# Performance work log

Measured on AMD Instinct MI355X. Metric: run time of the kernel, lower is better.

## Reference

```python
import jax, jax.numpy as jnp
import numpy as np

N_NODES = 10000
IN_CH = 512
HID = 128
HEADS = 4
OUT_CH = 256
N_EDGES = 160000
NEG_SLOPE = 0.2  # PyG GATConv default


def gat_conv(x, src, dst, W, a_src, a_dst, b):
    """PyG-style GATConv. x:[N,F_in], W:[F_in,H*C], a_src/a_dst:[H,C], b:[H*C].
    src/dst already include self-loops. Returns [N, H*C] (concat heads)."""
    N = x.shape[0]
    H, C = a_src.shape
    h = (x @ W).reshape(N, H, C)                     # [N,H,C]
    e_src = jnp.einsum('nhc,hc->nh', h, a_src)        # [N,H]
    e_dst = jnp.einsum('nhc,hc->nh', h, a_dst)
    alpha = jax.nn.leaky_relu(e_src[src] + e_dst[dst], NEG_SLOPE)  # [E,H]
    # softmax over incoming edges of each destination node
    m = jax.ops.segment_max(alpha, dst, num_segments=N)            # [N,H]
    ex = jnp.exp(alpha - m[dst])
    denom = jax.ops.segment_sum(ex, dst, num_segments=N)           # [N,H]
    coeff = ex / (denom[dst] + 1e-16)                              # [E,H]
    out = jax.ops.segment_sum(coeff[:, :, None] * h[src], dst, num_segments=N)  # [N,H,C]
    return out.reshape(N, H * C) + b


def _edges_with_self_loops(edge_index, n):
    loops = jnp.arange(n, dtype=edge_index.dtype)
    src = jnp.concatenate([edge_index[0], loops])
    dst = jnp.concatenate([edge_index[1], loops])
    return src, dst


def setup_inputs() -> dict:
    key = jax.random.key(0)
    ks = jax.random.split(key, 20)
    s = 0.05
    inp = {
        'x': jax.random.normal(ks[0], (N_NODES, IN_CH), jnp.float32),
        'W1': jax.random.normal(ks[1], (IN_CH, HEADS * HID), jnp.float32) * s,
        'a1s': jax.random.normal(ks[2], (HEADS, HID), jnp.float32) * s,
        'a1d': jax.random.normal(ks[3], (HEADS, HID), jnp.float32) * s,
        'b1': jnp.zeros((HEADS * HID,), jnp.float32),
        'W2': jax.random.normal(ks[4], (HEADS * HID, HEADS * HID), jnp.float32) * s,
        'a2s': jax.random.normal(ks[5], (HEADS, HID), jnp.float32) * s,
        'a2d': jax.random.normal(ks[6], (HEADS, HID), jnp.float32) * s,
        'b2': jnp.zeros((HEADS * HID,), jnp.float32),
        'W3': jax.random.normal(ks[7], (HEADS * HID, HID), jnp.float32) * s,
        'a3s': jax.random.normal(ks[8], (1, HID), jnp.float32) * s,
        'a3d': jax.random.normal(ks[9], (1, HID), jnp.float32) * s,
        'b3': jnp.zeros((HID,), jnp.float32),
        'Wl': jax.random.normal(ks[10], (HID, OUT_CH), jnp.float32) * s,
        'bl': jnp.zeros((OUT_CH,), jnp.float32),
        'Wr': jax.random.normal(ks[11], (IN_CH, OUT_CH), jnp.float32) * s,
        'br': jnp.zeros((OUT_CH,), jnp.float32),
        'edge_index': jax.random.randint(ks[12], (2, N_EDGES), 0, N_NODES, jnp.int64 if jax.config.jax_enable_x64 else jnp.int32),
    }
    return inp


def reference(x, W1, a1s, a1d, b1, W2, a2s, a2d, b2, W3, a3s, a3d, b3, Wl, bl, Wr, br, edge_index):
    src, dst = _edges_with_self_loops(edge_index, x.shape[0])
    residual = x @ Wr + br
    h = jax.nn.elu(gat_conv(x, src, dst, W1, a1s, a1d, b1))
    h = jax.nn.elu(gat_conv(h, src, dst, W2, a2s, a2d, b2))
    h = jax.nn.elu(gat_conv(h, src, dst, W3, a3s, a3d, b3))
    return h @ Wl + bl + residual
```

## Files before the change

kernel.cpp:

```cpp
#include <hip/hip_runtime.h>
#include <hip/hip_bf16.h>
#include <cstdint>
#include <cstddef>

#define N_NODES 10000
#define M_PAD   10112
#define HEADS   4

typedef __bf16 bfrag8 __attribute__((ext_vector_type(8)));
typedef __bf16 bfrag2 __attribute__((ext_vector_type(2)));
typedef float  floatx4 __attribute__((ext_vector_type(4)));
typedef float  floatx2 __attribute__((ext_vector_type(2)));

#define S0V (M_PAD * 512 / 8)
#define S1 (512 * 512)
#define S2 (512 * 512)
#define S3 (512 * 128)
#define S4 (128 * 256)
#define S5 (512 * 256)

__global__ __launch_bounds__(256) void prep(const float* __restrict__ x,
                                            const float* __restrict__ W1,
                                            const float* __restrict__ W2,
                                            const float* __restrict__ W3,
                                            const float* __restrict__ Wl,
                                            const float* __restrict__ Wr,
                                            const int* __restrict__ edst, int E,
                                            __bf16* __restrict__ xb,
                                            __bf16* __restrict__ W1T,
                                            __bf16* __restrict__ W2T,
                                            __bf16* __restrict__ W3T,
                                            __bf16* __restrict__ WlT,
                                            __bf16* __restrict__ WrT,
                                            int* __restrict__ deg) {
    int i = blockIdx.x * 256 + threadIdx.x;
    if (i < S0V) {
        int base = i * 8;
        int row = base >> 9;
        bfrag8 r = {};
        if (row < N_NODES) {
            float4 f0 = ((const float4*)x)[i * 2];
            float4 f1 = ((const float4*)x)[i * 2 + 1];
            r[0] = (__bf16)f0.x; r[1] = (__bf16)f0.y; r[2] = (__bf16)f0.z; r[3] = (__bf16)f0.w;
            r[4] = (__bf16)f1.x; r[5] = (__bf16)f1.y; r[6] = (__bf16)f1.z; r[7] = (__bf16)f1.w;
        }
        *(bfrag8*)(xb + base) = r;
    } else if ((i -= S0V) < S1) {
        int k = i >> 9, n = i & 511;
        W1T[n * 512 + k] = (__bf16)W1[i];
    } else if ((i -= S1) < S2) {
        int k = i >> 9, n = i & 511;
        W2T[n * 512 + k] = (__bf16)W2[i];
    } else if ((i -= S2) < S3) {
        int k = i >> 7, n = i & 127;
        W3T[n * 512 + k] = (__bf16)W3[i];
    } else if ((i -= S3) < S4) {
        int k = i >> 8, n = i & 255;
        WlT[n * 128 + k] = (__bf16)Wl[i];
    } else if ((i -= S4) < S5) {
        int k = i >> 8, n = i & 255;
        WrT[n * 512 + k] = (__bf16)Wr[i];
    } else if ((i -= S5) < E) {
        atomicAdd(&deg[edst[i]], 1);
    }
}


__global__ __launch_bounds__(256) void scan_kernel(const int* __restrict__ deg,
                                                   int* __restrict__ rowptr,
                                                   int* __restrict__ cursor, int n) {
    __shared__ int wtot[4], woff[4];
    int t = threadIdx.x, lane = t & 63, wv = t >> 6;
    int chunk = (n + 255) / 256;
    int beg = t * chunk, end = beg + chunk; if (end > n) end = n; if (beg > n) beg = n;
    int s = 0;
    for (int i = beg; i < end; ++i) s += deg[i] + 1;
    int v = s;
#pragma unroll
    for (int off = 1; off < 64; off <<= 1) {
        int o = __shfl_up(v, off);
        if (lane >= off) v += o;
    }
    if (lane == 63) wtot[wv] = v;
    __syncthreads();
    if (t == 0) {
        int r = 0;
#pragma unroll
        for (int i = 0; i < 4; ++i) { woff[i] = r; r += wtot[i]; }
        rowptr[n] = r;
    }
    __syncthreads();
    int off = woff[wv] + v - s;
    for (int i = beg; i < end; ++i) {
        rowptr[i] = off; cursor[i] = off;
        off += deg[i] + 1;
    }
}

__global__ __launch_bounds__(256) void scatter_kernel(const int* __restrict__ src,
                                                      const int* __restrict__ dst, int E, int n,
                                                      int* __restrict__ cursor,
                                                      int* __restrict__ csr) {
    int i = blockIdx.x * 256 + threadIdx.x;
    if (i < E) {
        int pos = atomicAdd(&cursor[dst[i]], 1);
        csr[pos] = src[i];
    } else if (i < E + n) {
        int v = i - E;
        int pos = atomicAdd(&cursor[v], 1);
        csr[pos] = v;
    }
}


template <int NT>
__device__ __forceinline__ void gemm_loop(const __bf16* __restrict__ A,
                                          const __bf16* __restrict__ BT, int K,
                                          int m0, int n0, int wave, int lane,
                                          __bf16* As, __bf16* Bs,
                                          floatx4 (&acc)[2][NT]) {
    int r = wave * 8 + (lane >> 3);
    int kof = (lane & 7) * 8;
    const __bf16* gA = A + (size_t)(m0 + r) * K + kof;
    const __bf16* gB = BT + (size_t)(n0 + r) * K + kof;
    __bf16* lA = As + r * 64 + kof;
    __bf16* lB = Bs + r * 64 + kof;
    const __bf16* fA = As + (wave * 32 + (lane & 15)) * 64 + (lane >> 4) * 8;
    const __bf16* fB = Bs + (lane & 15) * 64 + (lane >> 4) * 8;

    for (int k0 = 0; k0 < K; k0 += 64) {
#pragma unroll
        for (int u = 0; u < 4; ++u)
            __builtin_amdgcn_global_load_lds(
                (const __attribute__((address_space(1))) void*)(gA + (size_t)u * 32 * K),
                (__attribute__((address_space(3))) void*)(lA + u * 32 * 64), 16, 0, 0);
#pragma unroll
        for (int u = 0; u < NT / 2; ++u)
            __builtin_amdgcn_global_load_lds(
                (const __attribute__((address_space(1))) void*)(gB + (size_t)u * 32 * K),
                (__attribute__((address_space(3))) void*)(lB + u * 32 * 64), 16, 0, 0);
        gA += 64; gB += 64;
        __syncthreads();

#pragma unroll
        for (int ks = 0; ks < 2; ++ks) {
            bfrag8 a0 = *(const bfrag8*)(fA + ks * 32);
            bfrag8 a1 = *(const bfrag8*)(fA + 16 * 64 + ks * 32);
#pragma unroll
            for (int nt = 0; nt < NT; ++nt) {
                bfrag8 b = *(const bfrag8*)(fB + nt * 16 * 64 + ks * 32);
                acc[0][nt] = __builtin_amdgcn_mfma_f32_16x16x32_bf16(a0, b, acc[0][nt], 0, 0, 0);
                acc[1][nt] = __builtin_amdgcn_mfma_f32_16x16x32_bf16(a1, b, acc[1][nt], 0, 0, 0);
            }
        }
        __syncthreads();
    }
}

__global__ __launch_bounds__(256) void gemm_h(const __bf16* __restrict__ A,
                                              const __bf16* __restrict__ BT,
                                              unsigned char* __restrict__ C8,
                                              int N, int K, int H,
                                              const float* __restrict__ as_,
                                              const float* __restrict__ ad_,
                                              float* __restrict__ esp,
                                              float* __restrict__ edp) {
    __shared__ __align__(16) __bf16 As[128 * 64];
    __shared__ __align__(16) __bf16 Bs[64 * 64];
    int tid = threadIdx.x, wave = tid >> 6, lane = tid & 63;
    int n0 = blockIdx.x * 64, m0 = blockIdx.y * 128;
    floatx4 acc[2][4] = {};
    gemm_loop<4>(A, BT, K, m0, n0, wave, lane, As, Bs, acc);

    int crow = m0 + wave * 32 + (lane >> 4) * 4;
    int ccol = n0 + (lane & 15);
#pragma unroll
    for (int mt = 0; mt < 2; ++mt)
#pragma unroll
        for (int nt = 0; nt < 4; ++nt)
#pragma unroll
            for (int r = 0; r < 4; ++r) {
                float v = acc[mt][nt][r];
                size_t o = (size_t)(crow + mt * 16 + r) * N + ccol + nt * 16;
                int p = __builtin_amdgcn_cvt_pk_fp8_f32(v, v, 0, false);
                C8[o] = (unsigned char)(p & 0xff);
            }

    int head = n0 >> 7;
    int half = (n0 >> 6) & 1;
    float a_sv[4], a_dv[4];
#pragma unroll
    for (int nt = 0; nt < 4; ++nt) {
        int cin = (n0 & 64) + nt * 16 + (lane & 15);
        a_sv[nt] = as_[head * 128 + cin];
        a_dv[nt] = ad_[head * 128 + cin];
    }
    float* ep = esp + (size_t)half * M_PAD * H;
    float* dp = edp + (size_t)half * M_PAD * H;
#pragma unroll
    for (int mt = 0; mt < 2; ++mt)
#pragma unroll
        for (int r = 0; r < 4; ++r) {
            float ps = 0.f, pd = 0.f;
#pragma unroll
            for (int nt = 0; nt < 4; ++nt) {
                float v = acc[mt][nt][r];
                ps += v * a_sv[nt];
                pd += v * a_dv[nt];
            }
#pragma unroll
            for (int off = 8; off; off >>= 1) {
                ps += __shfl_xor(ps, off);
                pd += __shfl_xor(pd, off);
            }
            if ((lane & 15) == 0) {
                int row = crow + mt * 16 + r;
                ep[row * H + head] = ps;
                dp[row * H + head] = pd;
            }
        }
}

__global__ __launch_bounds__(256) void attn_reduce(const float* __restrict__ esp,
                                                   const float* __restrict__ edp,
                                                   float* __restrict__ es,
                                                   float* __restrict__ ed, int n, int H) {
    int i = blockIdx.x * 256 + threadIdx.x;
    if (i < n) {
        const int off = M_PAD * H;
        es[i] = esp[i] + esp[off + i];
        ed[i] = edp[i] + edp[off + i];
    }
}

__global__ __launch_bounds__(256) void gemm_final(const __bf16* __restrict__ A1,
                                                  const __bf16* __restrict__ B1T, int K1,
                                                  const __bf16* __restrict__ A2,
                                                  const __bf16* __restrict__ B2T, int K2,
                                                  float* __restrict__ C,
                                                  const float* __restrict__ bias1,
                                                  const float* __restrict__ bias2,
                                                  int M, int N) {
    __shared__ __align__(16) __bf16 As[128 * 64];
    __shared__ __align__(16) __bf16 Bs[64 * 64];
    int tid = threadIdx.x, wave = tid >> 6, lane = tid & 63;
    int n0 = blockIdx.x * 64, m0 = blockIdx.y * 128;
    floatx4 acc[2][4] = {};
    gemm_loop<4>(A1, B1T, K1, m0, n0, wave, lane, As, Bs, acc);
    gemm_loop<4>(A2, B2T, K2, m0, n0, wave, lane, As, Bs, acc);

    int crow = m0 + wave * 32 + (lane >> 4) * 4;
    int ccol = n0 + (lane & 15);
#pragma unroll
    for (int mt = 0; mt < 2; ++mt)
#pragma unroll
        for (int nt = 0; nt < 4; ++nt)
#pragma unroll
            for (int r = 0; r < 4; ++r) {
                int row = crow + mt * 16 + r;
                int col = ccol + nt * 16;
                if (row < M)
                    C[(size_t)row * N + col] = acc[mt][nt][r] + bias1[col] + bias2[col];
            }
}


template <int H>
__global__ __launch_bounds__(256) void gather_agg(const unsigned char* __restrict__ H8,
                                                  const float* __restrict__ es,
                                                  const float* __restrict__ ed,
                                                  const int* __restrict__ rowptr,
                                                  const int* __restrict__ csr,
                                                  const float* __restrict__ bias,
                                                  __bf16* __restrict__ outb) {
    constexpr int F = H * 128;
    constexpr int CH = F / 64;
    int wave = threadIdx.x >> 6, lane = threadIdx.x & 63;
    int node = blockIdx.x * 4 + wave;
    if (node >= M_PAD) return;
    int hsel = (H == 4) ? (lane >> 4) : 0;
    __bf16* op = outb + (size_t)node * F + lane * CH;
    if (node >= N_NODES) {
        if (H == 4) { bfrag8 z = {}; *(bfrag8*)op = z; }
        else        { bfrag2 z = {}; *(bfrag2*)op = z; }
        return;
    }
    const unsigned char* hp = H8 + lane * CH;
    float edv = ed[node * H + hsel];
    int beg = rowptr[node], end = rowptr[node + 1];
    float acc[CH] = {};
    float wsum = 0.f;
    int j = beg;
    for (; j + 7 < end; j += 8) {
        int s[8];
        float e[8];
#pragma unroll
        for (int u = 0; u < 8; ++u) s[u] = csr[j + u];
#pragma unroll
        for (int u = 0; u < 8; ++u) e[u] = es[s[u] * H + hsel];
        if (H == 4) {
            uint2 p[8];
#pragma unroll
            for (int u = 0; u < 8; ++u) p[u] = *(const uint2*)(hp + (size_t)s[u] * F);
#pragma unroll
            for (int u = 0; u < 8; ++u) {
                float t = e[u] + edv;
                t = t > 0.f ? t : 0.2f * t;
                float wgt = __expf(t);
                wsum += wgt;
                floatx2 f0 = __builtin_amdgcn_cvt_pk_f32_fp8(p[u].x, false);
                floatx2 f1 = __builtin_amdgcn_cvt_pk_f32_fp8(p[u].x, true);
                floatx2 f2 = __builtin_amdgcn_cvt_pk_f32_fp8(p[u].y, false);
                floatx2 f3 = __builtin_amdgcn_cvt_pk_f32_fp8(p[u].y, true);
                acc[0] += wgt * f0[0]; acc[1] += wgt * f0[1];
                acc[2] += wgt * f1[0]; acc[3] += wgt * f1[1];
                acc[4] += wgt * f2[0]; acc[5] += wgt * f2[1];
                acc[6] += wgt * f3[0]; acc[7] += wgt * f3[1];
            }
        } else {
            unsigned short p[8];
#pragma unroll
            for (int u = 0; u < 8; ++u) p[u] = *(const unsigned short*)(hp + (size_t)s[u] * F);
#pragma unroll
            for (int u = 0; u < 8; ++u) {
                float t = e[u] + edv;
                t = t > 0.f ? t : 0.2f * t;
                float wgt = __expf(t);
                wsum += wgt;
                floatx2 f0 = __builtin_amdgcn_cvt_pk_f32_fp8((int)p[u], false);
                acc[0] += wgt * f0[0]; acc[1] += wgt * f0[1];
            }
        }
    }
    for (; j < end; ++j) {
        int s0 = csr[j];
        float t = es[s0 * H + hsel] + edv;
        t = t > 0.f ? t : 0.2f * t;
        float wgt = __expf(t);
        wsum += wgt;
        if (H == 4) {
            uint2 p = *(const uint2*)(hp + (size_t)s0 * F);
            floatx2 f0 = __builtin_amdgcn_cvt_pk_f32_fp8(p.x, false);
            floatx2 f1 = __builtin_amdgcn_cvt_pk_f32_fp8(p.x, true);
            floatx2 f2 = __builtin_amdgcn_cvt_pk_f32_fp8(p.y, false);
            floatx2 f3 = __builtin_amdgcn_cvt_pk_f32_fp8(p.y, true);
            acc[0] += wgt * f0[0]; acc[1] += wgt * f0[1];
            acc[2] += wgt * f1[0]; acc[3] += wgt * f1[1];
            acc[4] += wgt * f2[0]; acc[5] += wgt * f2[1];
            acc[6] += wgt * f3[0]; acc[7] += wgt * f3[1];
        } else {
            unsigned short p = *(const unsigned short*)(hp + (size_t)s0 * F);
            floatx2 f0 = __builtin_amdgcn_cvt_pk_f32_fp8((int)p, false);
            acc[0] += wgt * f0[0]; acc[1] += wgt * f0[1];
        }
    }
    float inv = 1.f / (wsum + 1e-16f);
    if (H == 4) {
        bfrag8 r;
#pragma unroll
        for (int k = 0; k < 8; ++k) {
            float o = acc[k] * inv + bias[lane * 8 + k];
            o = o > 0.f ? o : __expf(o) - 1.f;
            r[k] = (__bf16)o;
        }
        *(bfrag8*)op = r;
    } else {
        bfrag2 r;
#pragma unroll
        for (int k = 0; k < 2; ++k) {
            float o = acc[k] * inv + bias[lane * 2 + k];
            o = o > 0.f ? o : __expf(o) - 1.f;
            r[k] = (__bf16)o;
        }
        *(bfrag2*)op = r;
    }
}


extern "C" void kernel_launch(void* const* d_in, const int* in_sizes, int n_in,
                              void* d_out, int out_size, void* d_ws, size_t ws_size,
                              hipStream_t stream) {
    const float* x   = (const float*)d_in[0];
    const float* W1  = (const float*)d_in[1];
    const float* a1s = (const float*)d_in[2];
    const float* a1d = (const float*)d_in[3];
    const float* b1  = (const float*)d_in[4];
    const float* W2  = (const float*)d_in[5];
    const float* a2s = (const float*)d_in[6];
    const float* a2d = (const float*)d_in[7];
    const float* b2  = (const float*)d_in[8];
    const float* W3  = (const float*)d_in[9];
    const float* a3s = (const float*)d_in[10];
    const float* a3d = (const float*)d_in[11];
    const float* b3  = (const float*)d_in[12];
    const float* Wl  = (const float*)d_in[13];
    const float* bl  = (const float*)d_in[14];
    const float* Wr  = (const float*)d_in[15];
    const float* br  = (const float*)d_in[16];
    const int*   ei  = (const int*)d_in[17];
    const int E = in_sizes[17] / 2;
    const int* esrc = ei;
    const int* edst = ei + E;
    const int slots = E + N_NODES;
    float* out = (float*)d_out;

    char* w = (char*)d_ws;
    auto alloc = [&](size_t b) { char* p = w; w += (b + 255) & ~(size_t)255; return p; };
    __bf16* xb  = (__bf16*)alloc((size_t)M_PAD * 512 * 2);
    __bf16* hb  = (__bf16*)alloc((size_t)M_PAD * 512 * 2);
    __bf16* hb3 = (__bf16*)alloc((size_t)M_PAD * 128 * 2);
    unsigned char* Hi8 = (unsigned char*)alloc((size_t)M_PAD * 512);
    __bf16* W1T = (__bf16*)alloc(512 * 512 * 2);
    __bf16* W2T = (__bf16*)alloc(512 * 512 * 2);
    __bf16* W3T = (__bf16*)alloc(128 * 512 * 2);
    __bf16* WlT = (__bf16*)alloc(256 * 128 * 2);
    __bf16* WrT = (__bf16*)alloc(256 * 512 * 2);
    float* es     = (float*)alloc(N_NODES * HEADS * 4);
    float* ed     = (float*)alloc(N_NODES * HEADS * 4);
    float* esp    = (float*)alloc((size_t)2 * M_PAD * HEADS * 4);
    float* edp    = (float*)alloc((size_t)2 * M_PAD * HEADS * 4);
    int*   deg    = (int*)alloc(N_NODES * 4);
    int*   rowptr = (int*)alloc((N_NODES + 1) * 4);
    int*   cursor = (int*)alloc(N_NODES * 4);
    int*   csr    = (int*)alloc((size_t)slots * 4);

    (void)hipMemsetAsync(deg, 0, N_NODES * sizeof(int), stream);

    const int sp_total = S0V + S1 + S2 + S3 + S4 + S5 + E;
    prep<<<(sp_total + 255) / 256, 256, 0, stream>>>(x, W1, W2, W3, Wl, Wr, edst, E,
                                                     xb, W1T, W2T, W3T, WlT, WrT, deg);
    scan_kernel<<<1, 256, 0, stream>>>(deg, rowptr, cursor, N_NODES);
    scatter_kernel<<<(E + N_NODES + 255) / 256, 256, 0, stream>>>(esrc, edst, E, N_NODES,
                                                                  cursor, csr);

    gemm_h<<<dim3(8, M_PAD / 128), 256, 0, stream>>>(xb, W1T, Hi8, 512, 512, 4,
                                                     a1s, a1d, esp, edp);
    attn_reduce<<<(N_NODES * 4 + 255) / 256, 256, 0, stream>>>(esp, edp, es, ed,
                                                               N_NODES * 4, 4);
    gather_agg<4><<<M_PAD / 4, 256, 0, stream>>>(Hi8, es, ed, rowptr, csr, b1, hb);
    gemm_h<<<dim3(8, M_PAD / 128), 256, 0, stream>>>(hb, W2T, Hi8, 512, 512, 4,
                                                     a2s, a2d, esp, edp);
    attn_reduce<<<(N_NODES * 4 + 255) / 256, 256, 0, stream>>>(esp, edp, es, ed,
                                                               N_NODES * 4, 4);
    gather_agg<4><<<M_PAD / 4, 256, 0, stream>>>(Hi8, es, ed, rowptr, csr, b2, hb);
    gemm_h<<<dim3(2, M_PAD / 128), 256, 0, stream>>>(hb, W3T, Hi8, 128, 512, 1,
                                                     a3s, a3d, esp, edp);
    attn_reduce<<<(N_NODES + 255) / 256, 256, 0, stream>>>(esp, edp, es, ed,
                                                           N_NODES, 1);
    gather_agg<1><<<M_PAD / 4, 256, 0, stream>>>(Hi8, es, ed, rowptr, csr, b3, hb3);
    gemm_final<<<dim3(4, M_PAD / 128), 256, 0, stream>>>(xb, WrT, 512, hb3, WlT, 128,
                                                         out, br, bl, N_NODES, 256);
}
```

Before: 272.7 us.

## Fold attention partial-sum reduction into gather and vectorize weight transposes

```diff
diff --git a/kernel.cpp b/kernel.cpp
--- a/kernel.cpp
+++ b/kernel.cpp
@@ -13,11 +13,11 @@
 typedef float  floatx2 __attribute__((ext_vector_type(2)));
 
 #define S0V (M_PAD * 512 / 8)
-#define S1 (512 * 512)
-#define S2 (512 * 512)
-#define S3 (512 * 128)
-#define S4 (128 * 256)
-#define S5 (512 * 256)
+#define S1E (512 * 512 / 8)
+#define S2E (512 * 512 / 8)
+#define S3E (512 * 128 / 8)
+#define S4E (128 * 256 / 8)
+#define S5E (512 * 256 / 8)
 
 __global__ __launch_bounds__(256) void prep(const float* __restrict__ x,
                                             const float* __restrict__ W1,
@@ -45,22 +45,37 @@
             r[4] = (__bf16)f1.x; r[5] = (__bf16)f1.y; r[6] = (__bf16)f1.z; r[7] = (__bf16)f1.w;
         }
         *(bfrag8*)(xb + base) = r;
-    } else if ((i -= S0V) < S1) {
-        int k = i >> 9, n = i & 511;
-        W1T[n * 512 + k] = (__bf16)W1[i];
-    } else if ((i -= S1) < S2) {
-        int k = i >> 9, n = i & 511;
-        W2T[n * 512 + k] = (__bf16)W2[i];
-    } else if ((i -= S2) < S3) {
-        int k = i >> 7, n = i & 127;
-        W3T[n * 512 + k] = (__bf16)W3[i];
-    } else if ((i -= S3) < S4) {
-        int k = i >> 8, n = i & 255;
-        WlT[n * 128 + k] = (__bf16)Wl[i];
-    } else if ((i -= S4) < S5) {
-        int k = i >> 8, n = i & 255;
-        WrT[n * 512 + k] = (__bf16)Wr[i];
-    } else if ((i -= S5) < E) {
+    } else if ((i -= S0V) < S1E) {
+        int n = i & 511, kb = (i >> 9) * 8;
+        bfrag8 r;
+#pragma unroll
+        for (int t = 0; t < 8; ++t) r[t] = (__bf16)W1[(kb + t) * 512 + n];
+        *(bfrag8*)(W1T + n * 512 + kb) = r;
+    } else if ((i -= S1E) < S2E) {
+        int n = i & 511, kb = (i >> 9) * 8;
+        bfrag8 r;
+#pragma unroll
+        for (int t = 0; t < 8; ++t) r[t] = (__bf16)W2[(kb + t) * 512 + n];
+        *(bfrag8*)(W2T + n * 512 + kb) = r;
+    } else if ((i -= S2E) < S3E) {
+        int n = i & 127, kb = (i >> 7) * 8;
+        bfrag8 r;
+#pragma unroll
+        for (int t = 0; t < 8; ++t) r[t] = (__bf16)W3[(kb + t) * 128 + n];
+        *(bfrag8*)(W3T + n * 512 + kb) = r;
+    } else if ((i -= S3E) < S4E) {
+        int n = i & 255, kb = (i >> 8) * 8;
+        bfrag8 r;
+#pragma unroll
+        for (int t = 0; t < 8; ++t) r[t] = (__bf16)Wl[(kb + t) * 256 + n];
+        *(bfrag8*)(WlT + n * 128 + kb) = r;
+    } else if ((i -= S4E) < S5E) {
+        int n = i & 255, kb = (i >> 8) * 8;
+        bfrag8 r;
+#pragma unroll
+        for (int t = 0; t < 8; ++t) r[t] = (__bf16)Wr[(kb + t) * 256 + n];
+        *(bfrag8*)(WrT + n * 512 + kb) = r;
+    } else if ((i -= S5E) < E) {
         atomicAdd(&deg[edst[i]], 1);
     }
 }
@@ -219,18 +234,6 @@
                 dp[row * H + head] = pd;
             }
         }
-}
-
-__global__ __launch_bounds__(256) void attn_reduce(const float* __restrict__ esp,
-                                                   const float* __restrict__ edp,
-                                                   float* __restrict__ es,
-                                                   float* __restrict__ ed, int n, int H) {
-    int i = blockIdx.x * 256 + threadIdx.x;
-    if (i < n) {
-        const int off = M_PAD * H;
-        es[i] = esp[i] + esp[off + i];
-        ed[i] = edp[i] + edp[off + i];
-    }
 }
 
 __global__ __launch_bounds__(256) void gemm_final(const __bf16* __restrict__ A1,
@@ -267,14 +270,15 @@
 
 template <int H>
 __global__ __launch_bounds__(256) void gather_agg(const unsigned char* __restrict__ H8,
-                                                  const float* __restrict__ es,
-                                                  const float* __restrict__ ed,
+                                                  const float* __restrict__ esp,
+                                                  const float* __restrict__ edp,
                                                   const int* __restrict__ rowptr,
                                                   const int* __restrict__ csr,
                                                   const float* __restrict__ bias,
                                                   __bf16* __restrict__ outb) {
     constexpr int F = H * 128;
     constexpr int CH = F / 64;
+    constexpr int PO = M_PAD * H;
     int wave = threadIdx.x >> 6, lane = threadIdx.x & 63;
     int node = blockIdx.x * 4 + wave;
     if (node >= M_PAD) return;
@@ -286,7 +290,7 @@
         return;
     }
     const unsigned char* hp = H8 + lane * CH;
-    float edv = ed[node * H + hsel];
+    float edv = edp[node * H + hsel] + edp[PO + node * H + hsel];
     int beg = rowptr[node], end = rowptr[node + 1];
     float acc[CH] = {};
     float wsum = 0.f;
@@ -297,7 +301,8 @@
 #pragma unroll
         for (int u = 0; u < 8; ++u) s[u] = csr[j + u];
 #pragma unroll
-        for (int u = 0; u < 8; ++u) e[u] = es[s[u] * H + hsel];
+        for (int u = 0; u < 8; ++u)
+            e[u] = esp[s[u] * H + hsel] + esp[PO + s[u] * H + hsel];
         if (H == 4) {
             uint2 p[8];
 #pragma unroll
@@ -334,7 +339,7 @@
     }
     for (; j < end; ++j) {
         int s0 = csr[j];
-        float t = es[s0 * H + hsel] + edv;
+        float t = esp[s0 * H + hsel] + esp[PO + s0 * H + hsel] + edv;
         t = t > 0.f ? t : 0.2f * t;
         float wgt = __expf(t);
         wsum += wgt;
@@ -415,8 +420,6 @@
     __bf16* W3T = (__bf16*)alloc(128 * 512 * 2);
     __bf16* WlT = (__bf16*)alloc(256 * 128 * 2);
     __bf16* WrT = (__bf16*)alloc(256 * 512 * 2);
-    float* es     = (float*)alloc(N_NODES * HEADS * 4);
-    float* ed     = (float*)alloc(N_NODES * HEADS * 4);
     float* esp    = (float*)alloc((size_t)2 * M_PAD * HEADS * 4);
     float* edp    = (float*)alloc((size_t)2 * M_PAD * HEADS * 4);
     int*   deg    = (int*)alloc(N_NODES * 4);
@@ -426,7 +429,7 @@
 
     (void)hipMemsetAsync(deg, 0, N_NODES * sizeof(int), stream);
 
-    const int sp_total = S0V + S1 + S2 + S3 + S4 + S5 + E;
+    const int sp_total = S0V + S1E + S2E + S3E + S4E + S5E + E;
     prep<<<(sp_total + 255) / 256, 256, 0, stream>>>(x, W1, W2, W3, Wl, Wr, edst, E,
                                                      xb, W1T, W2T, W3T, WlT, WrT, deg);
     scan_kernel<<<1, 256, 0, stream>>>(deg, rowptr, cursor, N_NODES);
@@ -435,19 +438,13 @@
 
     gemm_h<<<dim3(8, M_PAD / 128), 256, 0, stream>>>(xb, W1T, Hi8, 512, 512, 4,
                                                      a1s, a1d, esp, edp);
-    attn_reduce<<<(N_NODES * 4 + 255) / 256, 256, 0, stream>>>(esp, edp, es, ed,
-                                                               N_NODES * 4, 4);
-    gather_agg<4><<<M_PAD / 4, 256, 0, stream>>>(Hi8, es, ed, rowptr, csr, b1, hb);
+    gather_agg<4><<<M_PAD / 4, 256, 0, stream>>>(Hi8, esp, edp, rowptr, csr, b1, hb);
     gemm_h<<<dim3(8, M_PAD / 128), 256, 0, stream>>>(hb, W2T, Hi8, 512, 512, 4,
                                                      a2s, a2d, esp, edp);
-    attn_reduce<<<(N_NODES * 4 + 255) / 256, 256, 0, stream>>>(esp, edp, es, ed,
-                                                               N_NODES * 4, 4);
-    gather_agg<4><<<M_PAD / 4, 256, 0, stream>>>(Hi8, es, ed, rowptr, csr, b2, hb);
+    gather_agg<4><<<M_PAD / 4, 256, 0, stream>>>(Hi8, esp, edp, rowptr, csr, b2, hb);
     gemm_h<<<dim3(2, M_PAD / 128), 256, 0, stream>>>(hb, W3T, Hi8, 128, 512, 1,
                                                      a3s, a3d, esp, edp);
-    attn_reduce<<<(N_NODES + 255) / 256, 256, 0, stream>>>(esp, edp, es, ed,
-                                                           N_NODES, 1);
-    gather_agg<1><<<M_PAD / 4, 256, 0, stream>>>(Hi8, es, ed, rowptr, csr, b3, hb3);
+    gather_agg<1><<<M_PAD / 4, 256, 0, stream>>>(Hi8, esp, edp, rowptr, csr, b3, hb3);
     gemm_final<<<dim3(4, M_PAD / 128), 256, 0, stream>>>(xb, WrT, 512, hb3, WlT, 128,
                                                          out, br, bl, N_NODES, 256);
 }
```

Measured after the change: 266.5 us. 1.02x faster.
